# Kernel optimization log

Measured on AMD Instinct MI355X. Metric: run time of the kernel, lower is better.

## Reference

```python
import jax, jax.numpy as jnp
import numpy as np

H, W = 85, 85
N_HEAD = 8

def layernorm(x, g, b, eps=1e-5):
    m = x.mean(-1, keepdims=True)
    v = ((x - m) ** 2).mean(-1, keepdims=True)
    return (x - m) * jax.lax.rsqrt(v + eps) * g + b


def setup_inputs() -> dict:
    key = jax.random.key(0)
    ks = jax.random.split(key, 12)
    B, C = 8, 256
    N = H * W
    hd = C // N_HEAD
    Ch = C * 4  # mlp_ratio = 4
    init = lambda k, fan_in, sh: (jax.random.normal(k, sh, jnp.float32) / np.float32(np.sqrt(fan_in)))
    d = {}
    d['fx'] = jax.random.normal(ks[0], (B, N, C), jnp.float32)
    # ln_1
    d['ln1_g'] = jnp.ones((C,), jnp.float32); d['ln1_b'] = jnp.zeros((C,), jnp.float32)
    # Galerkin linear attention projections (per-head split of C)
    d['Wq'] = init(ks[1], C, (C, C)); d['bq'] = jnp.zeros((C,), jnp.float32)
    d['Wk'] = init(ks[2], C, (C, C)); d['bk'] = jnp.zeros((C,), jnp.float32)
    d['Wv'] = init(ks[3], C, (C, C)); d['bv'] = jnp.zeros((C,), jnp.float32)
    d['Wo'] = init(ks[4], C, (C, C)); d['bo'] = jnp.zeros((C,), jnp.float32)
    # per-head LayerNorms on K and V (Galerkin normalization replacing softmax)
    d['kln_g'] = jnp.ones((N_HEAD, hd), jnp.float32); d['kln_b'] = jnp.zeros((N_HEAD, hd), jnp.float32)
    d['vln_g'] = jnp.ones((N_HEAD, hd), jnp.float32); d['vln_b'] = jnp.zeros((N_HEAD, hd), jnp.float32)
    # ln_2
    d['ln2_g'] = jnp.ones((C,), jnp.float32); d['ln2_b'] = jnp.zeros((C,), jnp.float32)
    # MLP (n_layers=0, res=False): pre linear + gelu, post linear
    d['W1'] = init(ks[5], C, (C, Ch)); d['b1'] = jnp.zeros((Ch,), jnp.float32)
    d['W2'] = init(ks[6], Ch, (Ch, C)); d['b2'] = jnp.zeros((C,), jnp.float32)
    return d


def reference(fx, ln1_g, ln1_b, Wq, bq, Wk, bk, Wv, bv, Wo, bo,
              kln_g, kln_b, vln_g, vln_b, ln2_g, ln2_b, W1, b1, W2, b2):
    B, N, C = fx.shape
    hd = C // N_HEAD
    x = layernorm(fx, ln1_g, ln1_b)  # [B,N,C]
    # (permute/reshape to image grid and back is a no-op for per-token attention math)
    split = lambda t: t.reshape(B, N, N_HEAD, hd).transpose(0, 2, 1, 3)  # [B,h,N,d]
    q = split(x @ Wq + bq)
    k = split(x @ Wk + bk)
    v = split(x @ Wv + bv)
    # Galerkin: LayerNorm on K and V over head dim, no softmax
    k = layernorm(k, kln_g[None, :, None, :], kln_b[None, :, None, :])
    v = layernorm(v, vln_g[None, :, None, :], vln_b[None, :, None, :])
    kv = jnp.einsum('bhnd,bhne->bhde', k, v) / N  # [B,h,d,d]
    attn = jnp.einsum('bhnd,bhde->bhne', q, kv)   # [B,h,N,d]
    attn = attn.transpose(0, 2, 1, 3).reshape(B, N, C)
    attn = attn @ Wo + bo
    fx = fx + attn  # residual 1
    x2 = layernorm(fx, ln2_g, ln2_b)
    x2 = jax.nn.gelu(x2 @ W1 + b1) @ W2 + b2
    return fx + x2  # residual 2
```

## Files before the change

kernel.cpp:

```cpp
#include <hip/hip_runtime.h>
#include <hip/hip_bf16.h>
#include <stdint.h>

#define B_ 8
#define NTOK 7225
#define MTOT (B_*NTOK)
#define MROWS 58368
#define MT_FULL 226
#define MT_BATCH 29
#define MLP_TILES 904

typedef unsigned short u16;
typedef u16 u16x8 __attribute__((ext_vector_type(8)));
typedef u16 u16x4 __attribute__((ext_vector_type(4)));
typedef __bf16 bf16x8 __attribute__((ext_vector_type(8)));
typedef float f32x4 __attribute__((ext_vector_type(4)));

__device__ inline float bf2f(u16 u){ union{float f;uint32_t i;}c; c.i=((uint32_t)u)<<16; return c.f; }
__device__ inline u16 f2bf(float f){ union{float f;uint32_t i;}c; c.f=f; uint32_t x=c.i;
                                     return (u16)((x + 0x7fffu + ((x>>16)&1u))>>16); }
__device__ inline uint32_t cvt_pk_bf16(float a, float b){
  uint32_t r; asm("v_cvt_pk_bf16_f32 %0, %1, %2" : "=v"(r) : "v"(a), "v"(b)); return r;
}
__device__ inline float gelu_f(float x){
  float t = 0.7978845608028654f * x * (1.0f + 0.044715f*x*x);
  float e = __expf(2.0f*t);
  return x * (1.0f - __builtin_amdgcn_rcpf(e + 1.0f));
}

__device__ inline void gload_lds16(const u16* g, u16* l) {
  __builtin_amdgcn_global_load_lds(
      (__attribute__((address_space(1))) void*)(const_cast<u16*>(g)),
      (__attribute__((address_space(3))) void*)(l), 16, 0, 0);
}

template<int EPI>
__global__ __launch_bounds__(512, 2)
void gemm256(const u16* __restrict__ A, int lda,
             const u16* __restrict__ Bm, int ldb, long bStride,
             const float* __restrict__ bias, int biasStride,
             const float* __restrict__ res,
             void* __restrict__ outp, int ldo,
             int K, int rowsValid, int batchRowStride,
             const float* __restrict__ g2, const float* __restrict__ b2,
             u16* __restrict__ x2out)
{
  __shared__ alignas(16) u16 lds[65536];
  const int tid = threadIdx.x;
  const int wid = tid >> 6, lane = tid & 63;
  const int wm = wid >> 2, wn = wid & 3;

  const int gx = gridDim.x, gy = gridDim.y;
  const int n = gx * gy;
  const int flat = blockIdx.y * gx + blockIdx.x;
  const int qq = n >> 3, rr = n & 7;
  const int xcd = flat & 7, pos = flat >> 3;
  const int swz = (xcd < rr ? xcd*(qq+1) : rr*(qq+1) + (xcd-rr)*qq) + pos;
  const int bx = swz / gy, by = swz % gy;
  const int bz = blockIdx.z;

  const long rowBase = (long)bz * batchRowStride + (long)bx * 256;
  const int colBase = by * 256;
  const u16* Bp = Bm + (long)bz * bStride;
  const float* biasP = bias + bz * biasStride;

  const int srow = lane >> 2;
  const int scol = ((lane & 3) ^ ((lane >> 3) & 3)) * 8;
  const int NT = K >> 6;

  auto stageHalf = [&](int bf, int kt, int sel) {
    const int sub = sel >> 1;
    const int k0 = (kt << 6) + sub*32 + scol;
    u16* base = lds + ((sel & 1) ? 32768 : 0) + (bf*2 + sub)*8192;
#pragma unroll
    for (int i = 0; i < 2; ++i) {
      const int r0 = (wid*2 + i)*16;
      if ((sel & 1) == 0)
        gload_lds16(A + (rowBase + r0 + srow)*(long)lda + k0, base + r0*32);
      else
        gload_lds16(Bp + (long)(colBase + r0 + srow)*ldb + k0, base + r0*32);
    }
  };

  f32x4 acc[8][4] = {};
  bf16x8 afr[4], bfr[4];
  const int lr = lane & 15;
  const int sl = lane >> 4;
  const int sp = (sl ^ ((lr >> 1) & 3)) * 8;

  stageHalf(0, 0, 0); stageHalf(0, 0, 1); stageHalf(0, 0, 2); stageHalf(0, 0, 3);

  for (int kt = 0; kt < NT; ++kt) {
    const int bf = kt & 1;
    const bool st = (kt + 1 < NT);
#pragma unroll
    for (int ph = 0; ph < 4; ++ph) {
      const int sub = ph >> 1, mh = ph & 1;
      if (ph == 0) {
        asm volatile("s_waitcnt vmcnt(4)" ::: "memory");
      } else if (ph == 2) {
        if (kt == NT - 1) asm volatile("s_waitcnt vmcnt(0)" ::: "memory");
        else              asm volatile("s_waitcnt vmcnt(4)" ::: "memory");
      } else {
        asm volatile("s_waitcnt vmcnt(6)" ::: "memory");
      }
      __builtin_amdgcn_s_barrier();
      const u16* Ab = lds + (bf*2 + sub)*8192;
      const u16* Bb = lds + 32768 + (bf*2 + sub)*8192;
      if (mh == 0) {
#pragma unroll
        for (int ni = 0; ni < 4; ++ni)
          bfr[ni] = *reinterpret_cast<const bf16x8*>(&Bb[(wn*64 + ni*16 + lr)*32 + sp]);
      }
#pragma unroll
      for (int i = 0; i < 4; ++i)
        afr[i] = *reinterpret_cast<const bf16x8*>(&Ab[(wm*128 + (mh*4 + i)*16 + lr)*32 + sp]);
      if (st) stageHalf(bf ^ 1, kt + 1, ph);
      asm volatile("s_waitcnt lgkmcnt(0)" ::: "memory");
      __builtin_amdgcn_sched_barrier(0);
      __builtin_amdgcn_s_setprio(1);
#pragma unroll
      for (int i = 0; i < 4; ++i)
#pragma unroll
        for (int ni = 0; ni < 4; ++ni)
          acc[mh*4 + i][ni] =
              __builtin_amdgcn_mfma_f32_16x16x32_bf16(bfr[ni], afr[i], acc[mh*4 + i][ni], 0, 0, 0);
      __builtin_amdgcn_s_setprio(0);
    }
  }

  const int cq = sl * 4;
  {
    float* red = reinterpret_cast<float*>(lds);
    __syncthreads();
#pragma unroll
    for (int mi = 0; mi < 8; ++mi) {
      const int r = wm*128 + mi*16 + lr;
      const bool valid = (bx*256 + r < rowsValid);
      const long grow = rowBase + r;
      float s_r = 0.f, q_r = 0.f;
#pragma unroll
      for (int ni = 0; ni < 4; ++ni) {
        const int c0 = wn*64 + ni*16 + cq;
        f32x4 rv = valid ? *reinterpret_cast<const f32x4*>((const float*)res + grow*256 + c0)
                         : f32x4{0.f,0.f,0.f,0.f};
        f32x4 v = acc[mi][ni] + *reinterpret_cast<const f32x4*>(&biasP[c0]) + rv;
        acc[mi][ni] = v;
        s_r += v[0]+v[1]+v[2]+v[3];
        q_r += v[0]*v[0]+v[1]*v[1]+v[2]*v[2]+v[3]*v[3];
      }
      s_r += __shfl_xor(s_r, 16); s_r += __shfl_xor(s_r, 32);
      q_r += __shfl_xor(q_r, 16); q_r += __shfl_xor(q_r, 32);
      if (sl == 0) {
        red[       (wm*4 + wn)*128 + mi*16 + lr] = s_r;
        red[1024 + (wm*4 + wn)*128 + mi*16 + lr] = q_r;
      }
    }
    __syncthreads();
#pragma unroll
    for (int mi = 0; mi < 8; ++mi) {
      const int r = wm*128 + mi*16 + lr;
      if (bx*256 + r >= rowsValid) continue;
      const long grow = rowBase + r;
      const int rb = wm*4*128 + mi*16 + lr;
      float s_t = red[rb] + red[rb+128] + red[rb+256] + red[rb+384];
      float q_t = red[1024+rb] + red[1024+rb+128] + red[1024+rb+256] + red[1024+rb+384];
      const float m = s_t * (1.0f/256.0f);
      const float var = q_t * (1.0f/256.0f) - m*m;
      const float rs = rsqrtf(var + 1e-5f);
#pragma unroll
      for (int ni = 0; ni < 4; ++ni) {
        const int c0 = wn*64 + ni*16 + cq;
        const long oidx = grow*256 + c0;
        f32x4 v = acc[mi][ni];
        *reinterpret_cast<f32x4*>((float*)outp + oidx) = v;
        f32x4 gv = *reinterpret_cast<const f32x4*>(&g2[c0]);
        f32x4 bv = *reinterpret_cast<const f32x4*>(&b2[c0]);
        f32x4 xn = (v - m) * rs * gv + bv;
        uint2 pk; pk.x = cvt_pk_bf16(xn[0], xn[1]); pk.y = cvt_pk_bf16(xn[2], xn[3]);
        *reinterpret_cast<uint2*>(x2out + oidx) = pk;
      }
    }
  }
}

__global__ __launch_bounds__(512, 4)
void proj64(const u16* __restrict__ x2, const u16* __restrict__ Wt,
            const float* __restrict__ bias, u16* __restrict__ outp)
{
  __shared__ alignas(16) u16 Xs[16384];
  __shared__ alignas(16) u16 Wb[16384];
  __shared__ alignas(16) u16 Bb[4096];
  const int tid = threadIdx.x;
  const int wid = tid >> 6, lane = tid & 63;
  const int wm = wid >> 2, wn = wid & 3;
  const int lr = lane & 15, sl = lane >> 4;
  const long rowBase = (long)blockIdx.x * 64;

#pragma unroll
  for (int i = 0; i < 4; ++i) {
    const int u = i*512 + tid;
    const int r = u >> 5, pu = u & 31;
    gload_lds16(x2 + (rowBase + r)*256 + ((pu ^ (r & 31)) << 3), &Xs[u*8]);
  }
  auto stageW = [&](int c) {
#pragma unroll
    for (int i = 0; i < 4; ++i) {
      const int u = i*512 + tid;
      const int r = u >> 5, pu = u & 31;
      gload_lds16(Wt + (long)(c*64 + r)*256 + ((pu ^ (r & 31)) << 3), &Wb[u*8]);
    }
  };

  for (int c = 0; c < 8; ++c) {
    stageW(c);
    asm volatile("s_waitcnt vmcnt(0)" ::: "memory");
    __builtin_amdgcn_s_barrier();
    f32x4 acc[2] = {};
#pragma unroll
    for (int kk = 0; kk < 8; ++kk) {
      const int u = kk*4 + sl;
      const int rB = wn*16 + lr;
      bf16x8 wb = *reinterpret_cast<const bf16x8*>(&Wb[(rB*32 + (u ^ (rB & 31)))*8]);
#pragma unroll
      for (int mi = 0; mi < 2; ++mi) {
        const int rA = wm*32 + mi*16 + lr;
        bf16x8 xa = *reinterpret_cast<const bf16x8*>(&Xs[(rA*32 + (u ^ (rA & 31)))*8]);
        acc[mi] = __builtin_amdgcn_mfma_f32_16x16x32_bf16(wb, xa, acc[mi], 0, 0, 0);
      }
    }
#pragma unroll
    for (int mi = 0; mi < 2; ++mi) {
      const int r = wm*32 + mi*16 + lr;
      const int col = wn*16 + sl*4;
      f32x4 v = acc[mi] + *reinterpret_cast<const f32x4*>(&bias[c*64 + col]);
      uint2 pk; pk.x = cvt_pk_bf16(v[0], v[1]); pk.y = cvt_pk_bf16(v[2], v[3]);
      const int uw = (col >> 3) ^ (r & 7);
      *reinterpret_cast<uint2*>(&Bb[r*64 + uw*8 + (col & 7)]) = pk;
    }
    asm volatile("s_waitcnt lgkmcnt(0)" ::: "memory");
    __builtin_amdgcn_s_barrier();
    {
      const int r = tid >> 3, u = tid & 7;
      const int phys = u ^ (r & 7);
      u16x8 val = *reinterpret_cast<const u16x8*>(&Bb[r*64 + phys*8]);
      *reinterpret_cast<u16x8*>(outp + (rowBase + r)*512 + c*64 + u*8) = val;
    }
  }
}

__global__ __launch_bounds__(512, 4)
void mlp_fused4(const u16* __restrict__ x2, const u16* __restrict__ W1t,
                const u16* __restrict__ W2t, const float* __restrict__ b1,
                const float* __restrict__ b2, float* __restrict__ outF,
                int rowsValid)
{
  __shared__ alignas(16) u16 Xs[64*256];
  __shared__ alignas(16) u16 Wb[16384];
  __shared__ alignas(16) u16 Hs[64*64];
  const int tid = threadIdx.x;
  const int wid = tid >> 6, lane = tid & 63;
  const int wm = wid >> 2, wn = wid & 3;
  const int lr = lane & 15, sl = lane >> 4;
  const long rowBase = (long)blockIdx.x * 64;

#pragma unroll
  for (int i = 0; i < 4; ++i) {
    const int u = i*512 + tid;
    const int r = u >> 5, pu = u & 31;
    gload_lds16(x2 + (rowBase + r)*256 + ((pu ^ (r & 31)) << 3), &Xs[u*8]);
  }
  auto stageW1 = [&](int c) {
#pragma unroll
    for (int i = 0; i < 4; ++i) {
      const int u = i*512 + tid;
      const int r = u >> 5, pu = u & 31;
      gload_lds16(W1t + (long)(c*64 + r)*256 + ((pu ^ (r & 31)) << 3), &Wb[u*8]);
    }
  };
  auto stageW2 = [&](int c) {
#pragma unroll
    for (int i = 0; i < 4; ++i) {
      const int u = i*512 + tid;
      const int r = u >> 3, pu = u & 7;
      gload_lds16(W2t + (long)r*1024 + c*64 + ((pu ^ (r & 7)) << 3), &Wb[u*8]);
    }
  };
  stageW1(0);
  asm volatile("s_waitcnt vmcnt(0)" ::: "memory");
  __syncthreads();

  f32x4 acc2[2][4] = {};
  for (int c = 0; c < 16; ++c) {
    f32x4 acc1[2] = {};
#pragma unroll
    for (int kk = 0; kk < 8; ++kk) {
      const int u = kk*4 + sl;
      const int rB = wn*16 + lr;
      bf16x8 wb = *reinterpret_cast<const bf16x8*>(&Wb[(rB*32 + (u ^ (rB & 31)))*8]);
#pragma unroll
      for (int mi = 0; mi < 2; ++mi) {
        const int rA = wm*32 + mi*16 + lr;
        bf16x8 xa = *reinterpret_cast<const bf16x8*>(&Xs[(rA*32 + (u ^ (rA & 31)))*8]);
        acc1[mi] = __builtin_amdgcn_mfma_f32_16x16x32_bf16(wb, xa, acc1[mi], 0, 0, 0);
      }
    }
    const float* b1c = b1 + c*64;
#pragma unroll
    for (int mi = 0; mi < 2; ++mi) {
      const int r = wm*32 + mi*16 + lr;
      const int col = wn*16 + sl*4;
      f32x4 v = acc1[mi] + *reinterpret_cast<const f32x4*>(&b1c[col]);
      uint2 pk; pk.x = cvt_pk_bf16(gelu_f(v[0]), gelu_f(v[1]));
      pk.y = cvt_pk_bf16(gelu_f(v[2]), gelu_f(v[3]));
      const int uw = (col >> 3) ^ (r & 7);
      *reinterpret_cast<uint2*>(&Hs[r*64 + uw*8 + (col & 7)]) = pk;
    }
    asm volatile("s_waitcnt lgkmcnt(0)" ::: "memory");
    __builtin_amdgcn_s_barrier();
    stageW2(c);
    asm volatile("s_waitcnt vmcnt(0)" ::: "memory");
    __builtin_amdgcn_s_barrier();

#pragma unroll
    for (int kk2 = 0; kk2 < 2; ++kk2) {
      const int u = kk2*4 + sl;
      bf16x8 ha[2];
#pragma unroll
      for (int mi = 0; mi < 2; ++mi) {
        const int r = wm*32 + mi*16 + lr;
        ha[mi] = *reinterpret_cast<const bf16x8*>(&Hs[(r*8 + (u ^ (r & 7)))*8]);
      }
#pragma unroll
      for (int nj = 0; nj < 4; ++nj) {
        const int rB = wn*64 + nj*16 + lr;
        bf16x8 wb = *reinterpret_cast<const bf16x8*>(&Wb[(rB*8 + (u ^ (rB & 7)))*8]);
#pragma unroll
        for (int mi = 0; mi < 2; ++mi)
          acc2[mi][nj] = __builtin_amdgcn_mfma_f32_16x16x32_bf16(wb, ha[mi], acc2[mi][nj], 0, 0, 0);
      }
    }
    __builtin_amdgcn_s_barrier();
    if (c + 1 < 16) {
      stageW1(c + 1);
      asm volatile("s_waitcnt vmcnt(0)" ::: "memory");
      __builtin_amdgcn_s_barrier();
    }
  }
#pragma unroll
  for (int mi = 0; mi < 2; ++mi) {
    const int r = wm*32 + mi*16 + lr;
    if (rowBase + r < rowsValid) {
      float* orow = outF + (rowBase + r)*256;
#pragma unroll
      for (int nj = 0; nj < 4; ++nj) {
        const int col = wn*64 + nj*16 + sl*4;
        f32x4 v = acc2[mi][nj] + *reinterpret_cast<const f32x4*>(&b2[col])
                + *reinterpret_cast<const f32x4*>(&orow[col]);
        *reinterpret_cast<f32x4*>(&orow[col]) = v;
      }
    }
  }
}

__global__ __launch_bounds__(256)
void ln_kernel(const float* __restrict__ in, const float* __restrict__ g,
               const float* __restrict__ bt, u16* __restrict__ out, int M)
{
  const int wv = threadIdx.x >> 6, lane = threadIdx.x & 63;
  const int t = blockIdx.x * 4 + wv;
  if (t >= M) return;
  const float4 x = reinterpret_cast<const float4*>(in + (long)t*256)[lane];
  float s = x.x + x.y + x.z + x.w;
  float q = x.x*x.x + x.y*x.y + x.z*x.z + x.w*x.w;
#pragma unroll
  for (int o = 32; o > 0; o >>= 1) { s += __shfl_xor(s, o); q += __shfl_xor(q, o); }
  const float m  = s * (1.0f/256.0f);
  const float var = q * (1.0f/256.0f) - m*m;
  const float rs = rsqrtf(var + 1e-5f);
  const float4 gv = reinterpret_cast<const float4*>(g)[lane];
  const float4 bv = reinterpret_cast<const float4*>(bt)[lane];
  uint2 o4;
  o4.x = cvt_pk_bf16((x.x - m)*rs*gv.x + bv.x, (x.y - m)*rs*gv.y + bv.y);
  o4.y = cvt_pk_bf16((x.z - m)*rs*gv.z + bv.z, (x.w - m)*rs*gv.w + bv.w);
  *reinterpret_cast<uint2*>(out + (long)t*256 + lane*4) = o4;
}

__global__ __launch_bounds__(256)
void kv_kernel(const u16* __restrict__ KV,
               const float* __restrict__ kg, const float* __restrict__ kb,
               const float* __restrict__ vg, const float* __restrict__ vb,
               float* __restrict__ kvout)
{
  const int bh = blockIdx.x, b = bh >> 3, h = bh & 7;
  const int tid = threadIdx.x;
  __shared__ u16 kls[256][32];
  __shared__ u16 vls[256][32];
  __shared__ float sg[4][32];
  if (tid < 32) {
    sg[0][tid] = kg[h*32 + tid];
    sg[1][tid] = kb[h*32 + tid];
    sg[2][tid] = vg[h*32 + tid];
    sg[3][tid] = vb[h*32 + tid];
  }
  const int d = tid >> 3, e0 = (tid & 7) * 4;
  float a0=0, a1=0, a2=0, a3=0;

  for (int sub = 0; sub < 2; ++sub) {
    const int r = blockIdx.y * 512 + sub * 256 + tid;
    __syncthreads();
    if (r < NTOK) {
      const u16* rowp = KV + (long)(b*NTOK + r)*512;
#pragma unroll
      for (int kv2 = 0; kv2 < 2; ++kv2) {
        const u16* p = rowp + (kv2 ? 256 : 0) + h*32;
        float xv[32]; float s = 0.f;
#pragma unroll
        for (int q4 = 0; q4 < 4; ++q4) {
          u16x8 u = *reinterpret_cast<const u16x8*>(p + q4*8);
#pragma unroll
          for (int j = 0; j < 8; ++j) { float f = bf2f(u[j]); xv[q4*8+j] = f; s += f; }
        }
        const float m = s * (1.0f/32.0f);
        float vv = 0.f;
#pragma unroll
        for (int j = 0; j < 32; ++j) { float d2 = xv[j]-m; vv += d2*d2; }
        const float rs = rsqrtf(vv*(1.0f/32.0f) + 1e-5f);
        const float* gg = sg[kv2 ? 2 : 0];
        const float* bb = sg[kv2 ? 3 : 1];
        u16 (*dst)[32] = kv2 ? vls : kls;
#pragma unroll
        for (int j = 0; j < 32; ++j) dst[tid][j] = f2bf((xv[j]-m)*rs*gg[j] + bb[j]);
      }
    } else {
#pragma unroll
      for (int j = 0; j < 32; ++j) { kls[tid][j] = 0; vls[tid][j] = 0; }
    }
    __syncthreads();
#pragma unroll 4
    for (int rr = 0; rr < 256; ++rr) {
      const float kd = bf2f(kls[rr][d]);
      u16x4 v4 = *reinterpret_cast<const u16x4*>(&vls[rr][e0]);
      a0 += kd * bf2f(v4[0]); a1 += kd * bf2f(v4[1]);
      a2 += kd * bf2f(v4[2]); a3 += kd * bf2f(v4[3]);
    }
  }
  const float sc = 1.0f / (float)NTOK;
  float* o = kvout + (long)bh*1024 + d*32 + e0;
  atomicAdd(o+0, a0*sc); atomicAdd(o+1, a1*sc);
  atomicAdd(o+2, a2*sc); atomicAdd(o+3, a3*sc);
}

__global__ __launch_bounds__(256)
void woeff_kernel(const float* __restrict__ kv, const float* __restrict__ Wo,
                  u16* __restrict__ Woet)
{
  const int b = blockIdx.x >> 8, c = blockIdx.x & 255;
  const int rtid = threadIdx.x;
  const int h = rtid >> 5, dd = rtid & 31;
  const float* kvp = kv + ((long)(b*8 + h)*32 + dd)*32;
  float s = 0.f;
#pragma unroll 8
  for (int e = 0; e < 32; ++e) s += kvp[e] * Wo[(h*32 + e)*256 + c];
  Woet[(long)(b*256 + c)*256 + rtid] = f2bf(s);
}

__global__ __launch_bounds__(256)
void watt_kernel(const u16* __restrict__ wq_bf, const u16* __restrict__ Woet,
                 u16* __restrict__ Watt)
{
  const int b = blockIdx.x >> 8, c = blockIdx.x & 255;
  const int k = threadIdx.x;
  const u16* wr = wq_bf + (long)k*256;
  const u16* er = Woet + ((long)(b*256 + c))*256;
  float s = 0.f;
#pragma unroll 4
  for (int j0 = 0; j0 < 256; j0 += 8) {
    u16x8 wv = *reinterpret_cast<const u16x8*>(wr + j0);
    u16x8 ev = *reinterpret_cast<const u16x8*>(er + j0);
#pragma unroll
    for (int j = 0; j < 8; ++j) s += bf2f(wv[j]) * bf2f(ev[j]);
  }
  Watt[((long)(b*256 + c))*256 + k] = f2bf(s);
}

__global__ __launch_bounds__(256)
void be_kernel(const float* __restrict__ bq, const float* __restrict__ bo,
               const u16* __restrict__ Woet, float* __restrict__ be)
{
  const int b = blockIdx.x, c = threadIdx.x;
  const u16* er = Woet + ((long)(b*256 + c))*256;
  float s = bo[c];
#pragma unroll 4
  for (int j0 = 0; j0 < 256; j0 += 8) {
    u16x8 ev = *reinterpret_cast<const u16x8*>(er + j0);
#pragma unroll
    for (int j = 0; j < 8; ++j) s += bq[j0+j] * bf2f(ev[j]);
  }
  be[b*256 + c] = s;
}

__device__ void transpose_tile(const float* __restrict__ src, u16* __restrict__ dst,
                               int R, int C, int tcx, int trY)
{
  __shared__ float t[32][33];
  const int tc = tcx * 32, tr = trY * 32;
  const int lx = threadIdx.x & 31, ly = threadIdx.x >> 5;
#pragma unroll
  for (int i = 0; i < 32; i += 8)
    t[ly + i][lx] = src[(long)(tr + ly + i)*C + tc + lx];
  __syncthreads();
#pragma unroll
  for (int i = 0; i < 32; i += 8)
    dst[(long)(tc + ly + i)*R + tr + lx] = f2bf(t[lx][ly + i]);
}

__global__ __launch_bounds__(256)
void prep_kernel(const float* __restrict__ Wk, const float* __restrict__ Wv,
                 const float* __restrict__ W1, const float* __restrict__ W2,
                 const float* __restrict__ Wq,
                 const float* __restrict__ bk, const float* __restrict__ bv,
                 u16* __restrict__ Wkv_t, u16* __restrict__ W1_t, u16* __restrict__ W2_t,
                 u16* __restrict__ wq_bf, float* __restrict__ kvb, float* __restrict__ bkv)
{
  int b = blockIdx.x;
  if (b < 256)      { transpose_tile(W1, W1_t, 256, 1024, b & 31, b >> 5); }
  else if (b < 512) { b -= 256; transpose_tile(W2, W2_t, 1024, 256, b & 7, b >> 3); }
  else if (b < 576) { b -= 512; transpose_tile(Wk, Wkv_t,         256, 256, b & 7, b >> 3); }
  else if (b < 640) { b -= 576; transpose_tile(Wv, Wkv_t + 65536, 256, 256, b & 7, b >> 3); }
  else if (b < 648) {
    const int base = (b - 640) * 8192 + threadIdx.x;
#pragma unroll
    for (int i = 0; i < 32; ++i) wq_bf[base + i*256] = f2bf(Wq[base + i*256]);
  } else if (b < 656) {
    const int base = (b - 648) * 8192 + threadIdx.x;
#pragma unroll
    for (int i = 0; i < 32; ++i) kvb[base + i*256] = 0.f;
  } else {
    const int i = threadIdx.x;
    bkv[i] = bk[i]; bkv[256 + i] = bv[i];
  }
}

extern "C" void kernel_launch(void* const* d_in, const int* in_sizes, int n_in,
                              void* d_out, int out_size, void* d_ws, size_t ws_size,
                              hipStream_t stream)
{
  const float* fx    = (const float*)d_in[0];
  const float* ln1_g = (const float*)d_in[1];
  const float* ln1_b = (const float*)d_in[2];
  const float* Wq = (const float*)d_in[3];
  const float* bq = (const float*)d_in[4];
  const float* Wk = (const float*)d_in[5];
  const float* bk = (const float*)d_in[6];
  const float* Wv = (const float*)d_in[7];
  const float* bv = (const float*)d_in[8];
  const float* Wo = (const float*)d_in[9];
  const float* bo = (const float*)d_in[10];
  const float* kg  = (const float*)d_in[11];
  const float* kbb = (const float*)d_in[12];
  const float* vg  = (const float*)d_in[13];
  const float* vbb = (const float*)d_in[14];
  const float* ln2_g = (const float*)d_in[15];
  const float* ln2_b = (const float*)d_in[16];
  const float* W1 = (const float*)d_in[17];
  const float* b1 = (const float*)d_in[18];
  const float* W2 = (const float*)d_in[19];
  const float* b2 = (const float*)d_in[20];
  float* outF = (float*)d_out;

  char* ws = (char*)d_ws;
  size_t off = 0;
  auto alloc = [&](size_t bytes) { char* p = ws + off; off += (bytes + 255) & ~(size_t)255; return p; };
  u16* bufX   = (u16*)alloc((size_t)MROWS*256*2);
  u16* bufKV  = (u16*)alloc((size_t)MROWS*512*2);
  u16* Wkv_t  = (u16*)alloc(512*256*2);
  u16* W1_t   = (u16*)alloc(1024*256*2);
  u16* W2_t   = (u16*)alloc(256*1024*2);
  u16* Woe_t  = (u16*)alloc((size_t)8*256*256*2);
  u16* Watt   = (u16*)alloc((size_t)8*256*256*2);
  u16* wq_bf  = (u16*)alloc(256*256*2);
  float* kvb  = (float*)alloc((size_t)64*1024*4);
  float* bkv  = (float*)alloc(512*4);
  float* be   = (float*)alloc(8*256*4);
  (void)ws_size; (void)out_size; (void)n_in; (void)in_sizes;

  prep_kernel<<<657, 256, 0, stream>>>(Wk, Wv, W1, W2, Wq, bk, bv,
                                       Wkv_t, W1_t, W2_t, wq_bf, kvb, bkv);

  ln_kernel<<<MTOT/4, 256, 0, stream>>>(fx, ln1_g, ln1_b, bufX, MTOT);

  proj64<<<MLP_TILES, 512, 0, stream>>>(bufX, Wkv_t, bkv, bufKV);

  kv_kernel<<<dim3(64, 15), 256, 0, stream>>>(bufKV, kg, kbb, vg, vbb, kvb);

  woeff_kernel<<<2048, 256, 0, stream>>>(kvb, Wo, Woe_t);
  watt_kernel<<<2048, 256, 0, stream>>>(wq_bf, Woe_t, Watt);
  be_kernel<<<8, 256, 0, stream>>>(bq, bo, Woe_t, be);

  gemm256<3><<<dim3(MT_BATCH, 1, 8), 512, 0, stream>>>(
      bufX, 256, Watt, 256, 65536, be, 256, fx, outF, 256, 256, NTOK, NTOK,
      ln2_g, ln2_b, bufX);

  mlp_fused4<<<MLP_TILES, 512, 0, stream>>>(bufX, W1_t, W2_t, b1, b2, outF, MTOT);
}
```

Baseline: 293.7 us.

## Replace 256-row attention-output GEMM with 64-row tiles fused with LayerNorm

Swaps the 256x256-tile attention-output GEMM for a new kernel that handles 64 rows per block and loops over four 64-column chunks of W_att. That raises the grid from 232 blocks to 904 at higher occupancy, so the GPU's compute units are less underfilled. The kernel still fuses bias, residual and LayerNorm-2 in the epilogue. It now keeps the pre-norm values as bf16 in registers and normalizes those rounded values, which adds a small precision loss. It also stages the full weight chunk per pass, adding redundant weight reloads across blocks.

```diff
diff --git a/kernel.cpp b/kernel.cpp
--- a/kernel.cpp
+++ b/kernel.cpp
@@ -6,9 +6,8 @@
 #define NTOK 7225
 #define MTOT (B_*NTOK)
 #define MROWS 58368
-#define MT_FULL 226
-#define MT_BATCH 29
 #define MLP_TILES 904
+#define ATT_TILES 113
 
 typedef unsigned short u16;
 typedef u16 u16x8 __attribute__((ext_vector_type(8)));
@@ -32,156 +31,6 @@
   __builtin_amdgcn_global_load_lds(
       (__attribute__((address_space(1))) void*)(const_cast<u16*>(g)),
       (__attribute__((address_space(3))) void*)(l), 16, 0, 0);
-}
-
-template<int EPI>
-__global__ __launch_bounds__(512, 2)
-void gemm256(const u16* __restrict__ A, int lda,
-             const u16* __restrict__ Bm, int ldb, long bStride,
-             const float* __restrict__ bias, int biasStride,
-             const float* __restrict__ res,
-             void* __restrict__ outp, int ldo,
-             int K, int rowsValid, int batchRowStride,
-             const float* __restrict__ g2, const float* __restrict__ b2,
-             u16* __restrict__ x2out)
-{
-  __shared__ alignas(16) u16 lds[65536];
-  const int tid = threadIdx.x;
-  const int wid = tid >> 6, lane = tid & 63;
-  const int wm = wid >> 2, wn = wid & 3;
-
-  const int gx = gridDim.x, gy = gridDim.y;
-  const int n = gx * gy;
-  const int flat = blockIdx.y * gx + blockIdx.x;
-  const int qq = n >> 3, rr = n & 7;
-  const int xcd = flat & 7, pos = flat >> 3;
-  const int swz = (xcd < rr ? xcd*(qq+1) : rr*(qq+1) + (xcd-rr)*qq) + pos;
-  const int bx = swz / gy, by = swz % gy;
-  const int bz = blockIdx.z;
-
-  const long rowBase = (long)bz * batchRowStride + (long)bx * 256;
-  const int colBase = by * 256;
-  const u16* Bp = Bm + (long)bz * bStride;
-  const float* biasP = bias + bz * biasStride;
-
-  const int srow = lane >> 2;
-  const int scol = ((lane & 3) ^ ((lane >> 3) & 3)) * 8;
-  const int NT = K >> 6;
-
-  auto stageHalf = [&](int bf, int kt, int sel) {
-    const int sub = sel >> 1;
-    const int k0 = (kt << 6) + sub*32 + scol;
-    u16* base = lds + ((sel & 1) ? 32768 : 0) + (bf*2 + sub)*8192;
-#pragma unroll
-    for (int i = 0; i < 2; ++i) {
-      const int r0 = (wid*2 + i)*16;
-      if ((sel & 1) == 0)
-        gload_lds16(A + (rowBase + r0 + srow)*(long)lda + k0, base + r0*32);
-      else
-        gload_lds16(Bp + (long)(colBase + r0 + srow)*ldb + k0, base + r0*32);
-    }
-  };
-
-  f32x4 acc[8][4] = {};
-  bf16x8 afr[4], bfr[4];
-  const int lr = lane & 15;
-  const int sl = lane >> 4;
-  const int sp = (sl ^ ((lr >> 1) & 3)) * 8;
-
-  stageHalf(0, 0, 0); stageHalf(0, 0, 1); stageHalf(0, 0, 2); stageHalf(0, 0, 3);
-
-  for (int kt = 0; kt < NT; ++kt) {
-    const int bf = kt & 1;
-    const bool st = (kt + 1 < NT);
-#pragma unroll
-    for (int ph = 0; ph < 4; ++ph) {
-      const int sub = ph >> 1, mh = ph & 1;
-      if (ph == 0) {
-        asm volatile("s_waitcnt vmcnt(4)" ::: "memory");
-      } else if (ph == 2) {
-        if (kt == NT - 1) asm volatile("s_waitcnt vmcnt(0)" ::: "memory");
-        else              asm volatile("s_waitcnt vmcnt(4)" ::: "memory");
-      } else {
-        asm volatile("s_waitcnt vmcnt(6)" ::: "memory");
-      }
-      __builtin_amdgcn_s_barrier();
-      const u16* Ab = lds + (bf*2 + sub)*8192;
-      const u16* Bb = lds + 32768 + (bf*2 + sub)*8192;
-      if (mh == 0) {
-#pragma unroll
-        for (int ni = 0; ni < 4; ++ni)
-          bfr[ni] = *reinterpret_cast<const bf16x8*>(&Bb[(wn*64 + ni*16 + lr)*32 + sp]);
-      }
-#pragma unroll
-      for (int i = 0; i < 4; ++i)
-        afr[i] = *reinterpret_cast<const bf16x8*>(&Ab[(wm*128 + (mh*4 + i)*16 + lr)*32 + sp]);
-      if (st) stageHalf(bf ^ 1, kt + 1, ph);
-      asm volatile("s_waitcnt lgkmcnt(0)" ::: "memory");
-      __builtin_amdgcn_sched_barrier(0);
-      __builtin_amdgcn_s_setprio(1);
-#pragma unroll
-      for (int i = 0; i < 4; ++i)
-#pragma unroll
-        for (int ni = 0; ni < 4; ++ni)
-          acc[mh*4 + i][ni] =
-              __builtin_amdgcn_mfma_f32_16x16x32_bf16(bfr[ni], afr[i], acc[mh*4 + i][ni], 0, 0, 0);
-      __builtin_amdgcn_s_setprio(0);
-    }
-  }
-
-  const int cq = sl * 4;
-  {
-    float* red = reinterpret_cast<float*>(lds);
-    __syncthreads();
-#pragma unroll
-    for (int mi = 0; mi < 8; ++mi) {
-      const int r = wm*128 + mi*16 + lr;
-      const bool valid = (bx*256 + r < rowsValid);
-      const long grow = rowBase + r;
-      float s_r = 0.f, q_r = 0.f;
-#pragma unroll
-      for (int ni = 0; ni < 4; ++ni) {
-        const int c0 = wn*64 + ni*16 + cq;
-        f32x4 rv = valid ? *reinterpret_cast<const f32x4*>((const float*)res + grow*256 + c0)
-                         : f32x4{0.f,0.f,0.f,0.f};
-        f32x4 v = acc[mi][ni] + *reinterpret_cast<const f32x4*>(&biasP[c0]) + rv;
-        acc[mi][ni] = v;
-        s_r += v[0]+v[1]+v[2]+v[3];
-        q_r += v[0]*v[0]+v[1]*v[1]+v[2]*v[2]+v[3]*v[3];
-      }
-      s_r += __shfl_xor(s_r, 16); s_r += __shfl_xor(s_r, 32);
-      q_r += __shfl_xor(q_r, 16); q_r += __shfl_xor(q_r, 32);
-      if (sl == 0) {
-        red[       (wm*4 + wn)*128 + mi*16 + lr] = s_r;
-        red[1024 + (wm*4 + wn)*128 + mi*16 + lr] = q_r;
-      }
-    }
-    __syncthreads();
-#pragma unroll
-    for (int mi = 0; mi < 8; ++mi) {
-      const int r = wm*128 + mi*16 + lr;
-      if (bx*256 + r >= rowsValid) continue;
-      const long grow = rowBase + r;
-      const int rb = wm*4*128 + mi*16 + lr;
-      float s_t = red[rb] + red[rb+128] + red[rb+256] + red[rb+384];
-      float q_t = red[1024+rb] + red[1024+rb+128] + red[1024+rb+256] + red[1024+rb+384];
-      const float m = s_t * (1.0f/256.0f);
-      const float var = q_t * (1.0f/256.0f) - m*m;
-      const float rs = rsqrtf(var + 1e-5f);
-#pragma unroll
-      for (int ni = 0; ni < 4; ++ni) {
-        const int c0 = wn*64 + ni*16 + cq;
-        const long oidx = grow*256 + c0;
-        f32x4 v = acc[mi][ni];
-        *reinterpret_cast<f32x4*>((float*)outp + oidx) = v;
-        f32x4 gv = *reinterpret_cast<const f32x4*>(&g2[c0]);
-        f32x4 bv = *reinterpret_cast<const f32x4*>(&b2[c0]);
-        f32x4 xn = (v - m) * rs * gv + bv;
-        uint2 pk; pk.x = cvt_pk_bf16(xn[0], xn[1]); pk.y = cvt_pk_bf16(xn[2], xn[3]);
-        *reinterpret_cast<uint2*>(x2out + oidx) = pk;
-      }
-    }
-  }
 }
 
 __global__ __launch_bounds__(512, 4)
@@ -245,6 +94,119 @@
       const int phys = u ^ (r & 7);
       u16x8 val = *reinterpret_cast<const u16x8*>(&Bb[r*64 + phys*8]);
       *reinterpret_cast<u16x8*>(outp + (rowBase + r)*512 + c*64 + u*8) = val;
+    }
+  }
+}
+
+__global__ __launch_bounds__(512, 4)
+void att64(const u16* __restrict__ x2, const u16* __restrict__ Watt,
+           const float* __restrict__ be, const float* __restrict__ fx,
+           float* __restrict__ outF, u16* __restrict__ x2out,
+           const float* __restrict__ g2, const float* __restrict__ b2)
+{
+  __shared__ alignas(16) u16 Xs[16384];
+  __shared__ alignas(16) u16 Wb[16384];
+  __shared__ float Rb[512];
+  const int tid = threadIdx.x;
+  const int wid = tid >> 6, lane = tid & 63;
+  const int wm = wid >> 2, wn = wid & 3;
+  const int lr = lane & 15, sl = lane >> 4;
+  const int bx = blockIdx.x, bz = blockIdx.y;
+  const long rowBase = (long)bz * NTOK + (long)bx * 64;
+  const int rowsLeft = NTOK - bx * 64;
+  const u16* Wt = Watt + (long)bz * 65536;
+  const float* beP = be + bz * 256;
+
+#pragma unroll
+  for (int i = 0; i < 4; ++i) {
+    const int u = i*512 + tid;
+    const int r = u >> 5, pu = u & 31;
+    gload_lds16(x2 + (rowBase + r)*256 + ((pu ^ (r & 31)) << 3), &Xs[u*8]);
+  }
+  auto stageW = [&](int c) {
+#pragma unroll
+    for (int i = 0; i < 4; ++i) {
+      const int u = i*512 + tid;
+      const int r = u >> 5, pu = u & 31;
+      gload_lds16(Wt + (long)(c*64 + r)*256 + ((pu ^ (r & 31)) << 3), &Wb[u*8]);
+    }
+  };
+
+  uint2 pk[4][2];
+  float sacc[2] = {0.f, 0.f}, qacc[2] = {0.f, 0.f};
+
+#pragma unroll
+  for (int c = 0; c < 4; ++c) {
+    stageW(c);
+    asm volatile("s_waitcnt vmcnt(0)" ::: "memory");
+    __builtin_amdgcn_s_barrier();
+    f32x4 acc[2] = {};
+#pragma unroll
+    for (int kk = 0; kk < 8; ++kk) {
+      const int u = kk*4 + sl;
+      const int rB = wn*16 + lr;
+      bf16x8 wb = *reinterpret_cast<const bf16x8*>(&Wb[(rB*32 + (u ^ (rB & 31)))*8]);
+#pragma unroll
+      for (int mi = 0; mi < 2; ++mi) {
+        const int rA = wm*32 + mi*16 + lr;
+        bf16x8 xa = *reinterpret_cast<const bf16x8*>(&Xs[(rA*32 + (u ^ (rA & 31)))*8]);
+        acc[mi] = __builtin_amdgcn_mfma_f32_16x16x32_bf16(wb, xa, acc[mi], 0, 0, 0);
+      }
+    }
+#pragma unroll
+    for (int mi = 0; mi < 2; ++mi) {
+      const int r = wm*32 + mi*16 + lr;
+      const bool valid = (r < rowsLeft);
+      const int col = c*64 + wn*16 + sl*4;
+      const long oidx = (rowBase + r)*256 + col;
+      f32x4 rv = valid ? *reinterpret_cast<const f32x4*>(&fx[oidx])
+                       : f32x4{0.f,0.f,0.f,0.f};
+      f32x4 v = acc[mi] + *reinterpret_cast<const f32x4*>(&beP[col]) + rv;
+      if (valid) *reinterpret_cast<f32x4*>(&outF[oidx]) = v;
+      sacc[mi] += v[0]+v[1]+v[2]+v[3];
+      qacc[mi] += v[0]*v[0]+v[1]*v[1]+v[2]*v[2]+v[3]*v[3];
+      pk[c][mi].x = cvt_pk_bf16(v[0], v[1]);
+      pk[c][mi].y = cvt_pk_bf16(v[2], v[3]);
+    }
+    asm volatile("s_waitcnt lgkmcnt(0)" ::: "memory");
+    __builtin_amdgcn_s_barrier();
+  }
+
+#pragma unroll
+  for (int mi = 0; mi < 2; ++mi) {
+    float s = sacc[mi], q = qacc[mi];
+    s += __shfl_xor(s, 16); s += __shfl_xor(s, 32);
+    q += __shfl_xor(q, 16); q += __shfl_xor(q, 32);
+    if (sl == 0) {
+      const int r = wm*32 + mi*16 + lr;
+      Rb[      wn*64 + r] = s;
+      Rb[256 + wn*64 + r] = q;
+    }
+  }
+  __syncthreads();
+#pragma unroll
+  for (int mi = 0; mi < 2; ++mi) {
+    const int r = wm*32 + mi*16 + lr;
+    if (r >= rowsLeft) continue;
+    const float s_t = Rb[r] + Rb[64 + r] + Rb[128 + r] + Rb[192 + r];
+    const float q_t = Rb[256 + r] + Rb[320 + r] + Rb[384 + r] + Rb[448 + r];
+    const float m = s_t * (1.0f/256.0f);
+    const float var = q_t * (1.0f/256.0f) - m*m;
+    const float rs = rsqrtf(var + 1e-5f);
+    const long growb = (rowBase + r)*256;
+#pragma unroll
+    for (int c = 0; c < 4; ++c) {
+      const int col = c*64 + wn*16 + sl*4;
+      const f32x4 gv = *reinterpret_cast<const f32x4*>(&g2[col]);
+      const f32x4 bv = *reinterpret_cast<const f32x4*>(&b2[col]);
+      float v0 = bf2f((u16)(pk[c][mi].x & 0xffffu));
+      float v1 = bf2f((u16)(pk[c][mi].x >> 16));
+      float v2 = bf2f((u16)(pk[c][mi].y & 0xffffu));
+      float v3 = bf2f((u16)(pk[c][mi].y >> 16));
+      uint2 o;
+      o.x = cvt_pk_bf16((v0 - m)*rs*gv[0] + bv[0], (v1 - m)*rs*gv[1] + bv[1]);
+      o.y = cvt_pk_bf16((v2 - m)*rs*gv[2] + bv[2], (v3 - m)*rs*gv[3] + bv[3]);
+      *reinterpret_cast<uint2*>(x2out + growb + col) = o;
     }
   }
 }
@@ -598,9 +560,8 @@
   watt_kernel<<<2048, 256, 0, stream>>>(wq_bf, Woe_t, Watt);
   be_kernel<<<8, 256, 0, stream>>>(bq, bo, Woe_t, be);
 
-  gemm256<3><<<dim3(MT_BATCH, 1, 8), 512, 0, stream>>>(
-      bufX, 256, Watt, 256, 65536, be, 256, fx, outF, 256, 256, NTOK, NTOK,
-      ln2_g, ln2_b, bufX);
+  att64<<<dim3(ATT_TILES, 8), 512, 0, stream>>>(
+      bufX, Watt, be, fx, outF, bufX, ln2_g, ln2_b);
 
   mlp_fused4<<<MLP_TILES, 512, 0, stream>>>(bufX, W1_t, W2_t, b1, b2, outF, MTOT);
 }
```

Measured after the change: 294.2 us. No clear change (+0.2%).
